# Kernel optimization log

Hardware: AMD Instinct MI355X
Metric: run time of the kernel (lower is better)

Reference implementation:

```python
import jax, jax.numpy as jnp
import numpy as np

H1 = 768
H2 = 768
B, LQ, LK = 8, 1024, 1024


def setup_inputs() -> dict:
    key = jax.random.key(0)
    ks = jax.random.split(key, 12)
    s1 = 1.0 / np.sqrt(H1)
    s2 = 1.0 / np.sqrt(H2)
    # weights stored as [in, out] (equivalent to torch Linear weight.T)
    return {
        "tensor1": jax.random.normal(ks[0], (B, LQ, H1), jnp.float32),
        "tensor2": jax.random.normal(ks[1], (B, LK, H2), jnp.float32),
        "Wq": jax.random.uniform(ks[2], (3, H1, H2), jnp.float32, -s1, s1),
        "bq": jax.random.uniform(ks[3], (3, H2), jnp.float32, -s1, s1),
        "Wk": jax.random.uniform(ks[4], (3, H2, H2), jnp.float32, -s2, s2),
        "bk": jax.random.uniform(ks[5], (3, H2), jnp.float32, -s2, s2),
        "Wv": jax.random.uniform(ks[6], (3, H2, H2), jnp.float32, -s2, s2),
        "bv": jax.random.uniform(ks[7], (3, H2), jnp.float32, -s2, s2),
        "Wp": jax.random.uniform(ks[8], (3 * H2, H2), jnp.float32, -1.0 / np.sqrt(3 * H2), 1.0 / np.sqrt(3 * H2)),
        "bp": jax.random.uniform(ks[9], (H2,), jnp.float32, -1.0 / np.sqrt(3 * H2), 1.0 / np.sqrt(3 * H2)),
    }


def reference(tensor1, tensor2, Wq, bq, Wk, bk, Wv, bv, Wp, bp):
    # Three independent cross-attention heads, stacked on leading axis h=3.
    q = jnp.einsum("bqd,hde->hbqe", tensor1, Wq) + bq[:, None, None, :]  # [3,B,LQ,H2]
    k = jnp.einsum("bkd,hde->hbke", tensor2, Wk) + bk[:, None, None, :]  # [3,B,LK,H2]
    v = jnp.einsum("bkd,hde->hbke", tensor2, Wv) + bv[:, None, None, :]  # [3,B,LK,H2]
    scores = jnp.einsum("hbqe,hbke->hbqk", q, k)  # NOTE: no 1/sqrt(d) scaling, per original
    weights = jax.nn.softmax(scores, axis=-1)
    ctx = jnp.einsum("hbqk,hbke->hbqe", weights, v)  # [3,B,LQ,H2]
    # concat heads along feature dim -> [B,LQ,3*H2]
    multi = jnp.transpose(ctx, (1, 2, 0, 3)).reshape(ctx.shape[1], ctx.shape[2], -1)
    # project_multihead: ReLU then Linear
    return jax.nn.relu(multi) @ Wp + bp
```

## Files before the change

kernel.cpp:

```cpp
#include <hip/hip_runtime.h>
#include <hip/hip_bf16.h>


typedef _Float16 f16;
typedef __attribute__((ext_vector_type(8))) _Float16 f16x8;
typedef __attribute__((ext_vector_type(4))) float f32x4;
typedef __attribute__((ext_vector_type(4))) short s16x4;
typedef __attribute__((ext_vector_type(8))) short s16x8;

#define DI __device__ __forceinline__

DI short f2hs(float f){
  f16 h = (f16)f;
  return __builtin_bit_cast(short, h);
}
DI float hs2f(short s){
  return (float)__builtin_bit_cast(f16, s);
}

DI f32x4 mfma16(f16x8 a, f16x8 b, f32x4 c){
  return __builtin_amdgcn_mfma_f32_16x16x32_f16(a, b, c, 0, 0, 0);
}

#define GLL16(gp, lp) __builtin_amdgcn_global_load_lds( \
    (const __attribute__((address_space(1))) unsigned int*)(gp), \
    (__attribute__((address_space(3))) unsigned int*)(lp), 16, 0, 0)

__global__ void cvt2_f16_kernel(const float* __restrict__ a, const float* __restrict__ b,
                                short* __restrict__ oa, short* __restrict__ ob, int n4each){
  int i = blockIdx.x * blockDim.x + threadIdx.x;
  const float* in = (i < n4each) ? a : b;
  short* out = (i < n4each) ? oa : ob;
  int j = (i < n4each) ? i : i - n4each;
  f32x4 v = ((const f32x4*)in)[j];
  s16x4 o;
  o[0]=f2hs(v[0]); o[1]=f2hs(v[1]); o[2]=f2hs(v[2]); o[3]=f2hs(v[3]);
  ((s16x4*)out)[j] = o;
}

__global__ void transpose_cvt_kernel(const float* __restrict__ in, short* __restrict__ out, int R, int C){
  __shared__ float tile[32][33];
  long zoff = (long)blockIdx.z * R * C;
  in += zoff; out += zoff;
  int c0 = blockIdx.x * 32, r0 = blockIdx.y * 32;
  int tx = threadIdx.x, ty = threadIdx.y;
  #pragma unroll
  for (int k=0;k<4;k++)
    tile[ty + k*8][tx] = in[(long)(r0 + ty + k*8) * C + c0 + tx];
  __syncthreads();
  #pragma unroll
  for (int k=0;k<4;k++)
    out[(long)(c0 + ty + k*8) * R + r0 + tx] = f2hs(tile[tx][ty + k*8]);
}

DI void gemm_tile(const short* __restrict__ A, const short* __restrict__ Bt, int K,
                  int m0, int n0, short* As, short* Bs, f32x4 (&acc)[4][4])
{
  const int tid = threadIdx.x, wave = tid>>6, lane = tid&63;
  const int wm = wave>>1, wn = wave&1;
  const int fl = lane&15, fq = lane>>4;
  const int srow = lane>>2;
  const int scol = (((lane&3) ^ (srow&3)))*8;
  const int aswz = ((fq ^ (fl&3)))*8;
  for (int kk=0; kk<K; kk+=32){
    __syncthreads();
    #pragma unroll
    for (int r=0;r<2;r++){
      const int rb = r*64 + wave*16;
      GLL16(A  + (long)(m0+rb+srow)*K + kk + scol, As + rb*32);
      GLL16(Bt + (long)(n0+rb+srow)*K + kk + scol, Bs + rb*32);
    }
    __syncthreads();
    f16x8 a[4];
    #pragma unroll
    for (int i=0;i<4;i++) a[i] = *(const f16x8*)(As + (wm*64+i*16+fl)*32 + aswz);
    #pragma unroll
    for (int j=0;j<4;j++){
      f16x8 b = *(const f16x8*)(Bs + (wn*64+j*16+fl)*32 + aswz);
      #pragma unroll
      for (int i=0;i<4;i++) acc[i][j] = mfma16(a[i], b, acc[i][j]);
    }
  }
}

__global__ __launch_bounds__(256,2) void gemm_m_kernel(
    const short* __restrict__ WqH, const short* __restrict__ WkH, short* __restrict__ Mt)
{
  __shared__ short As[128*32];
  __shared__ short Bs[128*32];
  const int h = blockIdx.z;
  const int m0 = blockIdx.x*128, n0 = blockIdx.y*128;
  const int tid = threadIdx.x, wave = tid>>6, lane = tid&63;
  const int wm = wave>>1, wn = wave&1;
  const int fl = lane&15, fq = lane>>4;

  f32x4 vz = {0.f,0.f,0.f,0.f};
  f32x4 acc[4][4];
  #pragma unroll
  for (int i=0;i<4;i++)
    #pragma unroll
    for (int j=0;j<4;j++) acc[i][j] = vz;

  gemm_tile(WqH + (long)h*768*768, WkH + (long)h*768*768, 768, m0, n0, As, Bs, acc);

  short* outp = Mt + (long)h*768*768;
  #pragma unroll
  for (int j=0;j<4;j++){
    int col = n0 + wn*64 + j*16 + fl;
    #pragma unroll
    for (int i=0;i<4;i++){
      int row = m0 + wm*64 + i*16 + fq*4;
      s16x4 pack;
      #pragma unroll
      for (int r=0;r<4;r++) pack[r] = f2hs(acc[i][j][r]);
      *(s16x4*)(outp + (long)col*768 + row) = pack;
    }
  }
}

__global__ void vvec_kernel(const short* __restrict__ WkH, const float* __restrict__ bq,
                            float* __restrict__ w){
  const int h = blockIdx.x, chunk = blockIdx.y;
  const int tid = threadIdx.x, wave = tid>>6, lane = tid&63;
  const float* bql = bq + h*768 + lane*12;
  float bv[12];
  #pragma unroll
  for (int e=0;e<12;e++) bv[e] = bql[e];
  for (int r = 0; r < 24; r++){
    int d = chunk*96 + r*4 + wave;
    const short* row = WkH + ((long)h*768 + d)*768 + lane*12;
    float s = 0.f;
    #pragma unroll
    for (int e=0;e<12;e++) s += hs2f(row[e]) * bv[e];
    s += __shfl_xor(s, 1);
    s += __shfl_xor(s, 2);
    s += __shfl_xor(s, 4);
    s += __shfl_xor(s, 8);
    s += __shfl_xor(s, 16);
    s += __shfl_xor(s, 32);
    if (lane == 0) w[h*768 + d] = s;
  }
}

__global__ __launch_bounds__(256,2) void gemm_gv_kernel(
    const short* __restrict__ t1b, const short* __restrict__ t2b,
    const short* __restrict__ Mt, const short* __restrict__ WvT,
    const float* __restrict__ wv, const float* __restrict__ bv,
    short* __restrict__ Gb, short* __restrict__ Vtb)
{
  __shared__ short As[128*32];
  __shared__ short Bs[128*32];
  const int z = blockIdx.z;
  const int h = z % 3, which = z / 3;
  const short* A  = (which==0) ? t1b : t2b;
  const short* Bt = ((which==0)?Mt:WvT) + (long)h*768*768;
  const int m0 = blockIdx.x*128, n0 = blockIdx.y*128;
  const int tid = threadIdx.x, wave = tid>>6, lane = tid&63;
  const int wm = wave>>1, wn = wave&1;
  const int fl = lane&15, fq = lane>>4;

  f32x4 vz = {0.f,0.f,0.f,0.f};
  f32x4 acc[4][4];
  #pragma unroll
  for (int i=0;i<4;i++)
    #pragma unroll
    for (int j=0;j<4;j++) acc[i][j] = vz;

  gemm_tile(A, Bt, 768, m0, n0, As, Bs, acc);

  if (which == 0){
    const float* bias = wv + h*768;
    short* outp = Gb + (long)h*8192*768;
    #pragma unroll
    for (int j=0;j<4;j++){
      int col = n0 + wn*64 + j*16 + fl;
      float bb = bias[col];
      #pragma unroll
      for (int i=0;i<4;i++){
        int row = m0 + wm*64 + i*16 + fq*4;
        #pragma unroll
        for (int r=0;r<4;r++)
          outp[(long)(row+r)*768 + col] = f2hs(acc[i][j][r] + bb);
      }
    }
  } else {
    const float* bias = bv + h*768;
    const int bidx = m0 >> 10;
    const int lk0  = m0 & 1023;
    short* outp = Vtb + (long)(h*8 + bidx)*768*1024;
    #pragma unroll
    for (int j=0;j<4;j++){
      int e = n0 + wn*64 + j*16 + fl;
      float bb = bias[e];
      #pragma unroll
      for (int i=0;i<4;i++){
        int lk = lk0 + wm*64 + i*16 + fq*4;
        s16x4 pack;
        #pragma unroll
        for (int r=0;r<4;r++) pack[r] = f2hs(acc[i][j][r] + bb);
        *(s16x4*)(outp + (long)e*1024 + lk) = pack;
      }
    }
  }
}

__global__ __launch_bounds__(256,2) void qk_exp_kernel(
    const short* __restrict__ Gb, const short* __restrict__ t2b,
    short* __restrict__ P, float* __restrict__ Mx, float* __restrict__ Lx)
{
  __shared__ short As[128*32];
  __shared__ short Bs[128*32];
  __shared__ float red0[2][2][64];
  __shared__ float red1[2][2][64];
  const int id = blockIdx.x;
  const int xcd = id & 7, s_ = id >> 3;
  const int hb = xcd*3 + (s_ >> 6);
  const int inner = s_ & 63;
  const int qt = inner & 7, ct = inner >> 3;
  const int h = hb >> 3, b = hb & 7;
  const int tid = threadIdx.x, wave = tid>>6, lane = tid&63;
  const int wm = wave>>1, wn = wave&1;
  const int fl = lane&15, fq = lane>>4;
  const short* Abase = Gb + ((long)h*8192 + b*1024)*768;
  const short* Bbase = t2b + (long)b*1024*768;

  f32x4 vz = {0.f,0.f,0.f,0.f};
  f32x4 acc[4][4];
  #pragma unroll
  for (int i=0;i<4;i++)
    #pragma unroll
    for (int j=0;j<4;j++) acc[i][j] = vz;

  gemm_tile(Abase, Bbase, 768, qt*128, ct*128, As, Bs, acc);

  float mt[4][4];
  #pragma unroll
  for (int i=0;i<4;i++)
    #pragma unroll
    for (int r=0;r<4;r++){
      float m = acc[i][0][r];
      #pragma unroll
      for (int j=1;j<4;j++) m = fmaxf(m, acc[i][j][r]);
      m = fmaxf(m, __shfl_xor(m, 1));
      m = fmaxf(m, __shfl_xor(m, 2));
      m = fmaxf(m, __shfl_xor(m, 4));
      m = fmaxf(m, __shfl_xor(m, 8));
      mt[i][r] = m;
      if (fl == 0) red0[wn][wm][i*16 + fq*4 + r] = m;
    }
  __syncthreads();
  #pragma unroll
  for (int i=0;i<4;i++)
    #pragma unroll
    for (int r=0;r<4;r++)
      mt[i][r] = fmaxf(red0[0][wm][i*16 + fq*4 + r], red0[1][wm][i*16 + fq*4 + r]);

  #pragma unroll
  for (int i=0;i<4;i++)
    #pragma unroll
    for (int r=0;r<4;r++){
      float s = 0.f;
      #pragma unroll
      for (int j=0;j<4;j++){
        float p = __expf(acc[i][j][r] - mt[i][r]);
        acc[i][j][r] = p;
        s += p;
      }
      s += __shfl_xor(s, 1);
      s += __shfl_xor(s, 2);
      s += __shfl_xor(s, 4);
      s += __shfl_xor(s, 8);
      if (fl == 0) red1[wn][wm][i*16 + fq*4 + r] = s;
    }
  __syncthreads();

  #pragma unroll
  for (int j=0;j<4;j++){
    int c = ct*128 + wn*64 + j*16 + fl;
    #pragma unroll
    for (int i=0;i<4;i++){
      int q = qt*128 + wm*64 + i*16 + fq*4;
      #pragma unroll
      for (int r=0;r<4;r++)
        P[((long)hb*1024 + q + r)*1024 + c] = f2hs(acc[i][j][r]);
    }
  }
  if (fl == 0 && wn == 0){
    long aux = ((long)(hb*8 + ct))*1024 + qt*128;
    #pragma unroll
    for (int i=0;i<4;i++)
      #pragma unroll
      for (int r=0;r<4;r++){
        int row = wm*64 + i*16 + fq*4 + r;
        Mx[aux + row] = mt[i][r];
        Lx[aux + row] = red1[0][wm][row & 63] + red1[1][wm][row & 63];
      }
  }
}

__global__ void softmax_factor_kernel(const float* __restrict__ Mx, const float* __restrict__ Lx,
                                      short* __restrict__ Sc){
  int idx = blockIdx.x * 256 + threadIdx.x;
  int hb = idx >> 10, q = idx & 1023;
  float m[8], l[8];
  #pragma unroll
  for (int t=0;t<8;t++){
    long a = ((long)(hb*8 + t))*1024 + q;
    m[t] = Mx[a];
    l[t] = Lx[a];
  }
  float mg = m[0];
  #pragma unroll
  for (int t=1;t<8;t++) mg = fmaxf(mg, m[t]);
  float lg = 0.f;
  #pragma unroll
  for (int t=0;t<8;t++) lg += l[t] * __expf(m[t] - mg);
  float inv = 1.0f / lg;
  #pragma unroll
  for (int t=0;t<8;t++)
    Sc[((long)(hb*8 + t))*1024 + q] = f2hs(__expf(m[t] - mg) * inv);
}

__global__ __launch_bounds__(256,2) void pv_kernel(
    const short* __restrict__ P, const short* __restrict__ Vtb,
    const short* __restrict__ Sc, short* __restrict__ multi)
{
  __shared__ short As[128*32];
  __shared__ short Bs[128*32];
  const int id = blockIdx.x;
  const int xcd = id & 7, s_ = id >> 3;
  const int hb = xcd*3 + s_/48;
  const int inner = s_ % 48;
  const int qt = inner & 7, et = inner >> 3;
  const int h = hb >> 3, b = hb & 7;
  const int tid = threadIdx.x, wave = tid>>6, lane = tid&63;
  const int wm = wave>>1, wn = wave&1;
  const int fl = lane&15, fq = lane>>4;
  const int srow = lane>>2;
  const int scol = (((lane&3) ^ (srow&3)))*8;
  const int aswz = ((fq ^ (fl&3)))*8;
  const short* Abase = P + (long)hb*1024*1024 + (long)(qt*128)*1024;
  const short* Bbase = Vtb + (long)hb*768*1024 + (long)(et*128)*1024;
  const short* scp = Sc + (long)(hb*8)*1024 + qt*128;

  f32x4 vz = {0.f,0.f,0.f,0.f};
  f32x4 acc[4][4];
  #pragma unroll
  for (int i=0;i<4;i++)
    #pragma unroll
    for (int j=0;j<4;j++) acc[i][j] = vz;

  for (int ct=0; ct<8; ct++){
    f16 s[4];
    #pragma unroll
    for (int i=0;i<4;i++)
      s[i] = __builtin_bit_cast(f16, scp[ct*1024 + wm*64 + i*16 + fl]);
    #pragma unroll
    for (int t=0;t<4;t++){
      const int kk = ct*128 + t*32;
      __syncthreads();
      #pragma unroll
      for (int r=0;r<2;r++){
        const int rb = r*64 + wave*16;
        GLL16(Abase + (long)(rb+srow)*1024 + kk + scol, As + rb*32);
        GLL16(Bbase + (long)(rb+srow)*1024 + kk + scol, Bs + rb*32);
      }
      __syncthreads();
      f16x8 a[4];
      #pragma unroll
      for (int i=0;i<4;i++){
        f16x8 av = *(const f16x8*)(As + (wm*64+i*16+fl)*32 + aswz);
        f16x8 sv;
        #pragma unroll
        for (int e=0;e<8;e++) sv[e] = s[i];
        a[i] = av * sv;
      }
      #pragma unroll
      for (int j=0;j<4;j++){
        f16x8 bvv = *(const f16x8*)(Bs + (wn*64+j*16+fl)*32 + aswz);
        #pragma unroll
        for (int i=0;i<4;i++) acc[i][j] = mfma16(a[i], bvv, acc[i][j]);
      }
    }
  }

  short* mp = multi + (long)(b*1024 + qt*128)*2304 + h*768 + et*128;
  #pragma unroll
  for (int j=0;j<4;j++){
    int e = wn*64 + j*16 + fl;
    #pragma unroll
    for (int i=0;i<4;i++){
      int q = wm*64 + i*16 + fq*4;
      #pragma unroll
      for (int r=0;r<4;r++)
        mp[(long)(q+r)*2304 + e] = f2hs(fmaxf(acc[i][j][r], 0.f));
    }
  }
}

__global__ __launch_bounds__(256,2) void gemm_out_kernel(
    const short* __restrict__ A, const short* __restrict__ Bt,
    const float* __restrict__ bias, float* __restrict__ out)
{
  __shared__ short As[128*32];
  __shared__ short Bs[128*32];
  const int m0 = blockIdx.x*128, n0 = blockIdx.y*128;
  const int tid = threadIdx.x, wave = tid>>6, lane = tid&63;
  const int wm = wave>>1, wn = wave&1;
  const int fl = lane&15, fq = lane>>4;

  f32x4 vz = {0.f,0.f,0.f,0.f};
  f32x4 acc[4][4];
  #pragma unroll
  for (int i=0;i<4;i++)
    #pragma unroll
    for (int j=0;j<4;j++) acc[i][j] = vz;

  gemm_tile(A, Bt, 2304, m0, n0, As, Bs, acc);

  #pragma unroll
  for (int j=0;j<4;j++){
    int col = n0 + wn*64 + j*16 + fl;
    float bb = bias[col];
    #pragma unroll
    for (int i=0;i<4;i++){
      int row = m0 + wm*64 + i*16 + fq*4;
      #pragma unroll
      for (int r=0;r<4;r++)
        out[(long)(row+r)*768 + col] = acc[i][j][r] + bb;
    }
  }
}

extern "C" void kernel_launch(void* const* d_in, const int* in_sizes, int n_in,
                              void* d_out, int out_size, void* d_ws, size_t ws_size,
                              hipStream_t stream)
{
  const float* t1 = (const float*)d_in[0];
  const float* t2 = (const float*)d_in[1];
  const float* Wq = (const float*)d_in[2];
  const float* bq = (const float*)d_in[3];
  const float* Wk = (const float*)d_in[4];
  const float* Wv = (const float*)d_in[6];
  const float* bv = (const float*)d_in[7];
  const float* Wp = (const float*)d_in[8];
  const float* bp = (const float*)d_in[9];
  float* out = (float*)d_out;

  char* ws = (char*)d_ws;
  size_t off = 0;
  auto carve = [&](size_t bytes){ void* p = ws + off; off += (bytes + 255) & ~(size_t)255; return p; };
  short* t1b = (short*)carve(8L*1024*768*2);
  short* t2b = (short*)carve(8L*1024*768*2);
  short* WqH = (short*)carve(3L*768*768*2);
  short* WkH = (short*)carve(3L*768*768*2);
  short* WvT = (short*)carve(3L*768*768*2);
  short* WpT = (short*)carve(768L*2304*2);
  short* Mt  = (short*)carve(3L*768*768*2);
  short* Gb  = (short*)carve(3L*8192*768*2);
  short* Vtb = (short*)carve(3L*8*768*1024*2);
  short* Pb  = (short*)carve(24L*1024*1024*2);
  float* Mx  = (float*)carve(24L*8*1024*4);
  float* Lx  = (float*)carve(24L*8*1024*4);
  short* Scb = (short*)carve(24L*8*1024*2);
  float* wvb = (float*)carve(3L*768*4);
  short* multib = Gb;

  cvt2_f16_kernel<<<12288, 256, 0, stream>>>(t1, t2, t1b, t2b, 1572864);
  cvt2_f16_kernel<<<3456, 256, 0, stream>>>(Wq, Wk, WqH, WkH, 442368);
  transpose_cvt_kernel<<<dim3(24,24,3), dim3(32,8), 0, stream>>>(Wv, WvT, 768, 768);
  transpose_cvt_kernel<<<dim3(24,72,1), dim3(32,8), 0, stream>>>(Wp, WpT, 2304, 768);
  gemm_m_kernel<<<dim3(6,6,3), 256, 0, stream>>>(WqH, WkH, Mt);
  vvec_kernel<<<dim3(3,8), 256, 0, stream>>>(WkH, bq, wvb);
  gemm_gv_kernel<<<dim3(64,6,6), 256, 0, stream>>>(t1b, t2b, Mt, WvT, wvb, bv, Gb, Vtb);
  qk_exp_kernel<<<1536, 256, 0, stream>>>(Gb, t2b, Pb, Mx, Lx);
  softmax_factor_kernel<<<96, 256, 0, stream>>>(Mx, Lx, Scb);
  pv_kernel<<<1152, 256, 0, stream>>>(Pb, Vtb, Scb, multib);
  gemm_out_kernel<<<dim3(64,6,1), 256, 0, stream>>>(multib, WpT, bp, out);
}
```

Before: 422.3 us.

## Double GEMM K-step to 64, fuse softmax factors into PV, merge transposes

The shared GEMM tile loop now loads a K-slab of 64 (two 32-wide sub-tiles) per barrier pair instead of 32, halving the number of syncs per K step and doubling LDS use. The XOR swizzle on LDS layout is dropped, which may introduce bank conflicts on fragment reads. The softmax rescale-factor kernel is removed and its computation folded into the start of pv_kernel via shared memory. The two transpose launches are merged into one, and vvec now reads fp32 Wk directly so it no longer depends on the conversion ordering.

```diff
diff --git a/kernel.cpp b/kernel.cpp
--- a/kernel.cpp
+++ b/kernel.cpp
@@ -6,7 +6,6 @@
 typedef __attribute__((ext_vector_type(8))) _Float16 f16x8;
 typedef __attribute__((ext_vector_type(4))) float f32x4;
 typedef __attribute__((ext_vector_type(4))) short s16x4;
-typedef __attribute__((ext_vector_type(8))) short s16x8;
 
 #define DI __device__ __forceinline__
 
@@ -38,47 +37,57 @@
   ((s16x4*)out)[j] = o;
 }
 
-__global__ void transpose_cvt_kernel(const float* __restrict__ in, short* __restrict__ out, int R, int C){
+__global__ void transpose2_kernel(const float* __restrict__ Wv, const float* __restrict__ Wp,
+                                  short* __restrict__ WvT, short* __restrict__ WpT){
   __shared__ float tile[32][33];
-  long zoff = (long)blockIdx.z * R * C;
-  in += zoff; out += zoff;
-  int c0 = blockIdx.x * 32, r0 = blockIdx.y * 32;
+  const float* in; short* out; int R, r0;
+  if (blockIdx.z == 0){
+    int hd = blockIdx.y / 24;
+    in = Wv + (long)hd*768*768; out = WvT + (long)hd*768*768;
+    R = 768; r0 = (blockIdx.y % 24) * 32;
+  } else {
+    in = Wp; out = WpT; R = 2304; r0 = blockIdx.y * 32;
+  }
+  int c0 = blockIdx.x * 32;
   int tx = threadIdx.x, ty = threadIdx.y;
   #pragma unroll
   for (int k=0;k<4;k++)
-    tile[ty + k*8][tx] = in[(long)(r0 + ty + k*8) * C + c0 + tx];
+    tile[ty + k*8][tx] = in[(long)(r0 + ty + k*8) * 768 + c0 + tx];
   __syncthreads();
   #pragma unroll
   for (int k=0;k<4;k++)
     out[(long)(c0 + ty + k*8) * R + r0 + tx] = f2hs(tile[tx][ty + k*8]);
 }
 
-DI void gemm_tile(const short* __restrict__ A, const short* __restrict__ Bt, int K,
-                  int m0, int n0, short* As, short* Bs, f32x4 (&acc)[4][4])
-{
-  const int tid = threadIdx.x, wave = tid>>6, lane = tid&63;
-  const int wm = wave>>1, wn = wave&1;
-  const int fl = lane&15, fq = lane>>4;
-  const int srow = lane>>2;
-  const int scol = (((lane&3) ^ (srow&3)))*8;
-  const int aswz = ((fq ^ (fl&3)))*8;
-  for (int kk=0; kk<K; kk+=32){
+DI void gemm_tile64(const short* __restrict__ A, const short* __restrict__ Bt, int K,
+                    int m0, int n0, short* As, short* Bs, f32x4 (&acc)[4][4])
+{
+  const int tid = threadIdx.x, wave = tid>>6, lane = tid&63;
+  const int wm = wave>>1, wn = wave&1;
+  const int fl = lane&15, fq = lane>>4;
+  const int srow = lane>>2, scol = (lane&3)*8;
+  for (int kk=0; kk<K; kk+=64){
     __syncthreads();
     #pragma unroll
-    for (int r=0;r<2;r++){
-      const int rb = r*64 + wave*16;
-      GLL16(A  + (long)(m0+rb+srow)*K + kk + scol, As + rb*32);
-      GLL16(Bt + (long)(n0+rb+srow)*K + kk + scol, Bs + rb*32);
-    }
+    for (int c=0;c<2;c++)
+      #pragma unroll
+      for (int r=0;r<2;r++){
+        const int rb = r*64 + wave*16;
+        GLL16(A  + (long)(m0+rb+srow)*K + kk + c*32 + scol, As + c*4096 + rb*32);
+        GLL16(Bt + (long)(n0+rb+srow)*K + kk + c*32 + scol, Bs + c*4096 + rb*32);
+      }
     __syncthreads();
-    f16x8 a[4];
-    #pragma unroll
-    for (int i=0;i<4;i++) a[i] = *(const f16x8*)(As + (wm*64+i*16+fl)*32 + aswz);
-    #pragma unroll
-    for (int j=0;j<4;j++){
-      f16x8 b = *(const f16x8*)(Bs + (wn*64+j*16+fl)*32 + aswz);
-      #pragma unroll
-      for (int i=0;i<4;i++) acc[i][j] = mfma16(a[i], b, acc[i][j]);
+    #pragma unroll
+    for (int c=0;c<2;c++){
+      f16x8 a[4];
+      #pragma unroll
+      for (int i=0;i<4;i++) a[i] = *(const f16x8*)(As + c*4096 + (wm*64+i*16+fl)*32 + fq*8);
+      #pragma unroll
+      for (int j=0;j<4;j++){
+        f16x8 b = *(const f16x8*)(Bs + c*4096 + (wn*64+j*16+fl)*32 + fq*8);
+        #pragma unroll
+        for (int i=0;i<4;i++) acc[i][j] = mfma16(a[i], b, acc[i][j]);
+      }
     }
   }
 }
@@ -86,8 +95,8 @@
 __global__ __launch_bounds__(256,2) void gemm_m_kernel(
     const short* __restrict__ WqH, const short* __restrict__ WkH, short* __restrict__ Mt)
 {
-  __shared__ short As[128*32];
-  __shared__ short Bs[128*32];
+  __shared__ short As[8192];
+  __shared__ short Bs[8192];
   const int h = blockIdx.z;
   const int m0 = blockIdx.x*128, n0 = blockIdx.y*128;
   const int tid = threadIdx.x, wave = tid>>6, lane = tid&63;
@@ -101,7 +110,7 @@
     #pragma unroll
     for (int j=0;j<4;j++) acc[i][j] = vz;
 
-  gemm_tile(WqH + (long)h*768*768, WkH + (long)h*768*768, 768, m0, n0, As, Bs, acc);
+  gemm_tile64(WqH + (long)h*768*768, WkH + (long)h*768*768, 768, m0, n0, As, Bs, acc);
 
   short* outp = Mt + (long)h*768*768;
   #pragma unroll
@@ -118,7 +127,7 @@
   }
 }
 
-__global__ void vvec_kernel(const short* __restrict__ WkH, const float* __restrict__ bq,
+__global__ void vvec_kernel(const float* __restrict__ Wk, const float* __restrict__ bq,
                             float* __restrict__ w){
   const int h = blockIdx.x, chunk = blockIdx.y;
   const int tid = threadIdx.x, wave = tid>>6, lane = tid&63;
@@ -128,10 +137,10 @@
   for (int e=0;e<12;e++) bv[e] = bql[e];
   for (int r = 0; r < 24; r++){
     int d = chunk*96 + r*4 + wave;
-    const short* row = WkH + ((long)h*768 + d)*768 + lane*12;
+    const float* row = Wk + ((long)h*768 + d)*768 + lane*12;
     float s = 0.f;
     #pragma unroll
-    for (int e=0;e<12;e++) s += hs2f(row[e]) * bv[e];
+    for (int e=0;e<12;e++) s += row[e] * bv[e];
     s += __shfl_xor(s, 1);
     s += __shfl_xor(s, 2);
     s += __shfl_xor(s, 4);
@@ -148,8 +157,8 @@
     const float* __restrict__ wv, const float* __restrict__ bv,
     short* __restrict__ Gb, short* __restrict__ Vtb)
 {
-  __shared__ short As[128*32];
-  __shared__ short Bs[128*32];
+  __shared__ short As[8192];
+  __shared__ short Bs[8192];
   const int z = blockIdx.z;
   const int h = z % 3, which = z / 3;
   const short* A  = (which==0) ? t1b : t2b;
@@ -166,7 +175,7 @@
     #pragma unroll
     for (int j=0;j<4;j++) acc[i][j] = vz;
 
-  gemm_tile(A, Bt, 768, m0, n0, As, Bs, acc);
+  gemm_tile64(A, Bt, 768, m0, n0, As, Bs, acc);
 
   if (which == 0){
     const float* bias = wv + h*768;
@@ -208,8 +217,8 @@
     const short* __restrict__ Gb, const short* __restrict__ t2b,
     short* __restrict__ P, float* __restrict__ Mx, float* __restrict__ Lx)
 {
-  __shared__ short As[128*32];
-  __shared__ short Bs[128*32];
+  __shared__ short As[8192];
+  __shared__ short Bs[8192];
   __shared__ float red0[2][2][64];
   __shared__ float red1[2][2][64];
   const int id = blockIdx.x;
@@ -231,7 +240,7 @@
     #pragma unroll
     for (int j=0;j<4;j++) acc[i][j] = vz;
 
-  gemm_tile(Abase, Bbase, 768, qt*128, ct*128, As, Bs, acc);
+  gemm_tile64(Abase, Bbase, 768, qt*128, ct*128, As, Bs, acc);
 
   float mt[4][4];
   #pragma unroll
@@ -298,35 +307,13 @@
   }
 }
 
-__global__ void softmax_factor_kernel(const float* __restrict__ Mx, const float* __restrict__ Lx,
-                                      short* __restrict__ Sc){
-  int idx = blockIdx.x * 256 + threadIdx.x;
-  int hb = idx >> 10, q = idx & 1023;
-  float m[8], l[8];
-  #pragma unroll
-  for (int t=0;t<8;t++){
-    long a = ((long)(hb*8 + t))*1024 + q;
-    m[t] = Mx[a];
-    l[t] = Lx[a];
-  }
-  float mg = m[0];
-  #pragma unroll
-  for (int t=1;t<8;t++) mg = fmaxf(mg, m[t]);
-  float lg = 0.f;
-  #pragma unroll
-  for (int t=0;t<8;t++) lg += l[t] * __expf(m[t] - mg);
-  float inv = 1.0f / lg;
-  #pragma unroll
-  for (int t=0;t<8;t++)
-    Sc[((long)(hb*8 + t))*1024 + q] = f2hs(__expf(m[t] - mg) * inv);
-}
-
 __global__ __launch_bounds__(256,2) void pv_kernel(
     const short* __restrict__ P, const short* __restrict__ Vtb,
-    const short* __restrict__ Sc, short* __restrict__ multi)
-{
-  __shared__ short As[128*32];
-  __shared__ short Bs[128*32];
+    const float* __restrict__ Mx, const float* __restrict__ Lx, short* __restrict__ multi)
+{
+  __shared__ short As[8192];
+  __shared__ short Bs[8192];
+  __shared__ float scl[8][128];
   const int id = blockIdx.x;
   const int xcd = id & 7, s_ = id >> 3;
   const int hb = xcd*3 + s_/48;
@@ -336,12 +323,26 @@
   const int tid = threadIdx.x, wave = tid>>6, lane = tid&63;
   const int wm = wave>>1, wn = wave&1;
   const int fl = lane&15, fq = lane>>4;
-  const int srow = lane>>2;
-  const int scol = (((lane&3) ^ (srow&3)))*8;
-  const int aswz = ((fq ^ (fl&3)))*8;
+  const int srow = lane>>2, scol = (lane&3)*8;
   const short* Abase = P + (long)hb*1024*1024 + (long)(qt*128)*1024;
   const short* Bbase = Vtb + (long)hb*768*1024 + (long)(et*128)*1024;
-  const short* scp = Sc + (long)(hb*8)*1024 + qt*128;
+
+  if (tid < 128){
+    long a0 = ((long)(hb*8))*1024 + qt*128 + tid;
+    float m[8], l[8];
+    #pragma unroll
+    for (int t=0;t<8;t++){ m[t] = Mx[a0 + t*1024]; l[t] = Lx[a0 + t*1024]; }
+    float mg = m[0];
+    #pragma unroll
+    for (int t=1;t<8;t++) mg = fmaxf(mg, m[t]);
+    float lg = 0.f;
+    #pragma unroll
+    for (int t=0;t<8;t++) lg += l[t] * __expf(m[t] - mg);
+    float inv = 1.0f / lg;
+    #pragma unroll
+    for (int t=0;t<8;t++) scl[t][tid] = __expf(m[t] - mg) * inv;
+  }
+  __syncthreads();
 
   f32x4 vz = {0.f,0.f,0.f,0.f};
   f32x4 acc[4][4];
@@ -353,33 +354,37 @@
   for (int ct=0; ct<8; ct++){
     f16 s[4];
     #pragma unroll
-    for (int i=0;i<4;i++)
-      s[i] = __builtin_bit_cast(f16, scp[ct*1024 + wm*64 + i*16 + fl]);
-    #pragma unroll
-    for (int t=0;t<4;t++){
-      const int kk = ct*128 + t*32;
+    for (int i=0;i<4;i++) s[i] = (f16)scl[ct][wm*64 + i*16 + fl];
+    #pragma unroll
+    for (int t=0;t<2;t++){
+      const int kk = ct*128 + t*64;
       __syncthreads();
       #pragma unroll
-      for (int r=0;r<2;r++){
-        const int rb = r*64 + wave*16;
-        GLL16(Abase + (long)(rb+srow)*1024 + kk + scol, As + rb*32);
-        GLL16(Bbase + (long)(rb+srow)*1024 + kk + scol, Bs + rb*32);
-      }
+      for (int c=0;c<2;c++)
+        #pragma unroll
+        for (int r=0;r<2;r++){
+          const int rb = r*64 + wave*16;
+          GLL16(Abase + (long)(rb+srow)*1024 + kk + c*32 + scol, As + c*4096 + rb*32);
+          GLL16(Bbase + (long)(rb+srow)*1024 + kk + c*32 + scol, Bs + c*4096 + rb*32);
+        }
       __syncthreads();
-      f16x8 a[4];
-      #pragma unroll
-      for (int i=0;i<4;i++){
-        f16x8 av = *(const f16x8*)(As + (wm*64+i*16+fl)*32 + aswz);
-        f16x8 sv;
-        #pragma unroll
-        for (int e=0;e<8;e++) sv[e] = s[i];
-        a[i] = av * sv;
-      }
-      #pragma unroll
-      for (int j=0;j<4;j++){
-        f16x8 bvv = *(const f16x8*)(Bs + (wn*64+j*16+fl)*32 + aswz);
-        #pragma unroll
-        for (int i=0;i<4;i++) acc[i][j] = mfma16(a[i], bvv, acc[i][j]);
+      #pragma unroll
+      for (int c=0;c<2;c++){
+        f16x8 a[4];
+        #pragma unroll
+        for (int i=0;i<4;i++){
+          f16x8 av = *(const f16x8*)(As + c*4096 + (wm*64+i*16+fl)*32 + fq*8);
+          f16x8 sv;
+          #pragma unroll
+          for (int e=0;e<8;e++) sv[e] = s[i];
+          a[i] = av * sv;
+        }
+        #pragma unroll
+        for (int j=0;j<4;j++){
+          f16x8 bvv = *(const f16x8*)(Bs + c*4096 + (wn*64+j*16+fl)*32 + fq*8);
+          #pragma unroll
+          for (int i=0;i<4;i++) acc[i][j] = mfma16(a[i], bvv, acc[i][j]);
+        }
       }
     }
   }
@@ -402,8 +407,8 @@
     const short* __restrict__ A, const short* __restrict__ Bt,
     const float* __restrict__ bias, float* __restrict__ out)
 {
-  __shared__ short As[128*32];
-  __shared__ short Bs[128*32];
+  __shared__ short As[8192];
+  __shared__ short Bs[8192];
   const int m0 = blockIdx.x*128, n0 = blockIdx.y*128;
   const int tid = threadIdx.x, wave = tid>>6, lane = tid&63;
   const int wm = wave>>1, wn = wave&1;
@@ -416,7 +421,7 @@
     #pragma unroll
     for (int j=0;j<4;j++) acc[i][j] = vz;
 
-  gemm_tile(A, Bt, 2304, m0, n0, As, Bs, acc);
+  gemm_tile64(A, Bt, 2304, m0, n0, As, Bs, acc);
 
   #pragma unroll
   for (int j=0;j<4;j++){
@@ -462,19 +467,16 @@
   short* Pb  = (short*)carve(24L*1024*1024*2);
   float* Mx  = (float*)carve(24L*8*1024*4);
   float* Lx  = (float*)carve(24L*8*1024*4);
-  short* Scb = (short*)carve(24L*8*1024*2);
   float* wvb = (float*)carve(3L*768*4);
   short* multib = Gb;
 
   cvt2_f16_kernel<<<12288, 256, 0, stream>>>(t1, t2, t1b, t2b, 1572864);
   cvt2_f16_kernel<<<3456, 256, 0, stream>>>(Wq, Wk, WqH, WkH, 442368);
-  transpose_cvt_kernel<<<dim3(24,24,3), dim3(32,8), 0, stream>>>(Wv, WvT, 768, 768);
-  transpose_cvt_kernel<<<dim3(24,72,1), dim3(32,8), 0, stream>>>(Wp, WpT, 2304, 768);
+  transpose2_kernel<<<dim3(24,72,2), dim3(32,8), 0, stream>>>(Wv, Wp, WvT, WpT);
+  vvec_kernel<<<dim3(3,8), 256, 0, stream>>>(Wk, bq, wvb);
   gemm_m_kernel<<<dim3(6,6,3), 256, 0, stream>>>(WqH, WkH, Mt);
-  vvec_kernel<<<dim3(3,8), 256, 0, stream>>>(WkH, bq, wvb);
   gemm_gv_kernel<<<dim3(64,6,6), 256, 0, stream>>>(t1b, t2b, Mt, WvT, wvb, bv, Gb, Vtb);
   qk_exp_kernel<<<1536, 256, 0, stream>>>(Gb, t2b, Pb, Mx, Lx);
-  softmax_factor_kernel<<<96, 256, 0, stream>>>(Mx, Lx, Scb);
-  pv_kernel<<<1152, 256, 0, stream>>>(Pb, Vtb, Scb, multib);
+  pv_kernel<<<1152, 256, 0, stream>>>(Pb, Vtb, Mx, Lx, multib);
   gemm_out_kernel<<<dim3(64,6,1), 256, 0, stream>>>(multib, WpT, bp, out);
 }
```

New measurement: 405.8 us. 1.04x faster.
